# Kernel optimization log

Hardware: AMD Instinct MI355X
Metric: run time of the kernel (lower is better)

## Reference

```python
import jax, jax.numpy as jnp
import numpy as np

B, T, C, H = 4, 2048, 1024, 16
D = C // H  # head_size = 64

def setup_inputs() -> dict:
    key = jax.random.key(0)
    ks = jax.random.split(key, 9)
    s = 1.0 / np.sqrt(C)
    return {
        "x":  jax.random.normal(ks[0], (B, T, C), dtype=jnp.float32),
        "Wq": jax.random.normal(ks[1], (C, C), dtype=jnp.float32) * s,
        "bq": jnp.zeros((C,), dtype=jnp.float32),
        "Wk": jax.random.normal(ks[2], (C, C), dtype=jnp.float32) * s,
        "bk": jnp.zeros((C,), dtype=jnp.float32),
        "Wv": jax.random.normal(ks[3], (C, C), dtype=jnp.float32) * s,
        "bv": jnp.zeros((C,), dtype=jnp.float32),
        "Wp": jax.random.normal(ks[4], (C, C), dtype=jnp.float32) * s,
        "bp": jnp.zeros((C,), dtype=jnp.float32),
    }

def reference(x, Wq, bq, Wk, bk, Wv, bv, Wp, bp):
    # projections -> [B, H, T, D]
    def split_heads(y):
        return y.reshape(B, T, H, D).transpose(0, 2, 1, 3)
    q = split_heads(x @ Wq + bq)
    k = split_heads(x @ Wk + bk)
    v = split_heads(x @ Wv + bv)
    scale = 1.0 / np.sqrt(D)
    att = jnp.einsum('bhqd,bhkd->bhqk', q, k) * scale  # [B,H,T,T]
    causal = jnp.tril(jnp.ones((T, T), dtype=bool))
    att = jnp.where(causal, att, -jnp.inf)
    att = jax.nn.softmax(att, axis=-1)
    # dropout p=0.0 (eval): identity
    y = jnp.einsum('bhqk,bhkd->bhqd', att, v)  # [B,H,T,D]
    y = y.transpose(0, 2, 1, 3).reshape(B, T, C)
    return y @ Wp + bp
```

## Files before the change

kernel.cpp:

```cpp
#include <hip/hip_runtime.h>
#include <hip/hip_bf16.h>

#define B_ 4
#define T_ 2048
#define C_ 1024
#define H_ 16
#define D_ 64
#define M_ (B_*T_)

typedef __bf16 bf16x8 __attribute__((ext_vector_type(8)));
typedef float  f32x4  __attribute__((ext_vector_type(4)));
typedef float  f32x16 __attribute__((ext_vector_type(16)));

__device__ __forceinline__ unsigned short f2bf(float f) {
  unsigned u = __builtin_bit_cast(unsigned, f);
  u += 0x7FFF + ((u >> 16) & 1);
  return (unsigned short)(u >> 16);
}

__device__ __forceinline__ float exp2fast(float x) {
#if __has_builtin(__builtin_amdgcn_exp2f)
  return __builtin_amdgcn_exp2f(x);
#else
  float r; asm("v_exp_f32 %0, %1" : "=v"(r) : "v"(x)); return r;
#endif
}

__device__ __forceinline__ void gload_lds16(const void* g, void* l) {
  __builtin_amdgcn_global_load_lds(
      (const __attribute__((address_space(1))) void*)g,
      (__attribute__((address_space(3))) void*)l, 16, 0, 0);
}

__global__ void cvt_f32_bf16(const float* __restrict__ in,
                             unsigned short* __restrict__ out, int n4) {
  int i = blockIdx.x * blockDim.x + threadIdx.x;
  if (i < n4) {
    float4 v = ((const float4*)in)[i];
    ushort4 o;
    o.x = f2bf(v.x); o.y = f2bf(v.y); o.z = f2bf(v.z); o.w = f2bf(v.w);
    ((ushort4*)out)[i] = o;
  }
}

__global__ void transpose_cvt(const float* __restrict__ w0, const float* __restrict__ w1,
                              const float* __restrict__ w2, const float* __restrict__ w3,
                              unsigned short* __restrict__ tqkv,
                              unsigned short* __restrict__ tp) {
  __shared__ float tile[32][33];
  const float* src; unsigned short* dst;
  switch (blockIdx.z) {
    case 0: src = w0; dst = tqkv; break;
    case 1: src = w1; dst = tqkv + (size_t)C_ * C_; break;
    case 2: src = w2; dst = tqkv + (size_t)2 * C_ * C_; break;
    default: src = w3; dst = tp; break;
  }
  int bx = blockIdx.x * 32;
  int by = blockIdx.y * 32;
  int tx = threadIdx.x, ty = threadIdx.y;
  #pragma unroll
  for (int j = 0; j < 4; ++j)
    tile[ty + 8*j][tx] = src[(size_t)(by + ty + 8*j) * C_ + bx + tx];
  __syncthreads();
  #pragma unroll
  for (int j = 0; j < 4; ++j)
    dst[(size_t)(bx + ty + 8*j) * C_ + by + tx] = f2bf(tile[tx][ty + 8*j]);
}

__global__ __launch_bounds__(256, 2)
void gemm_qkv(const unsigned short* __restrict__ A,
              const unsigned short* __restrict__ Bt,
              const float* __restrict__ bq, const float* __restrict__ bk,
              const float* __restrict__ bv,
              unsigned short* __restrict__ qout, unsigned short* __restrict__ kout,
              unsigned short* __restrict__ vout, float qscale)
{
  __shared__ unsigned short lsA[128 * 64];
  __shared__ unsigned short lsB[128 * 64];
  const int wave = threadIdx.x >> 6;
  const int lane = threadIdx.x & 63;
  const int rowBase = blockIdx.y * 128;
  const int colBase = blockIdx.x * 128;
  const int rowOff = (wave >> 1) * 64;
  const int colOff = (wave & 1) * 64;
  const int lr = lane & 15;
  const int lg = lane >> 4;

  f32x4 acc[4][4] = {};

  const int chunkRow = lane >> 3;
  const int srcColE  = (((lane & 7) ^ (lane >> 3)) * 8);

  for (int k0 = 0; k0 < C_; k0 += 64) {
    #pragma unroll
    for (int c = 0; c < 4; ++c) {
      int chunk = c * 4 + wave;
      int r = chunk * 8 + chunkRow;
      gload_lds16(A  + (size_t)(rowBase + r) * C_ + k0 + srcColE, &lsA[chunk * 512]);
      gload_lds16(Bt + (size_t)(colBase + r) * C_ + k0 + srcColE, &lsB[chunk * 512]);
    }
    __syncthreads();
    #pragma unroll
    for (int kk = 0; kk < 2; ++kk) {
      bf16x8 af[4], bfr[4];
      const int kbyte = (kk * 32 + lg * 8) * 2;
      #pragma unroll
      for (int m = 0; m < 4; ++m) {
        int row = rowOff + m * 16 + lr;
        af[m] = *(const bf16x8*)((const char*)lsA + row * 128 + (kbyte ^ ((row & 7) << 4)));
      }
      #pragma unroll
      for (int n = 0; n < 4; ++n) {
        int row = colOff + n * 16 + lr;
        bfr[n] = *(const bf16x8*)((const char*)lsB + row * 128 + (kbyte ^ ((row & 7) << 4)));
      }
      #pragma unroll
      for (int m = 0; m < 4; ++m)
        #pragma unroll
        for (int n = 0; n < 4; ++n)
          acc[m][n] = __builtin_amdgcn_mfma_f32_16x16x32_bf16(af[m], bfr[n], acc[m][n], 0, 0, 0);
    }
    __syncthreads();
  }

  const int mid = colBase >> 10;
  const float* bias = (mid == 0) ? bq : (mid == 1) ? bk : bv;
  const float oscale = (mid == 0) ? qscale : 1.f;
  unsigned short* outp = (mid == 0) ? qout : (mid == 1) ? kout : vout;

  #pragma unroll
  for (int m = 0; m < 4; ++m) {
    int row0 = rowBase + rowOff + m * 16 + lg * 4;
    #pragma unroll
    for (int n = 0; n < 4; ++n) {
      int col = colBase + colOff + n * 16 + lr;
      int ncol = col & 1023;
      float bs = bias[ncol];
      int h = ncol >> 6, d = ncol & 63;
      if (mid == 2) {
        int b = row0 >> 11, t = row0 & 2047;
        int t2 = (t & ~12) | ((t & 4) << 1) | ((t & 8) >> 1);
        ushort4 o;
        o.x = f2bf(acc[m][n][0] + bs);
        o.y = f2bf(acc[m][n][1] + bs);
        o.z = f2bf(acc[m][n][2] + bs);
        o.w = f2bf(acc[m][n][3] + bs);
        *(ushort4*)(outp + (((size_t)b * H_ + h) * D_ + d) * T_ + t2) = o;
      } else {
        #pragma unroll
        for (int j = 0; j < 4; ++j) {
          int r = row0 + j;
          int b = r >> 11, t = r & 2047;
          outp[((((size_t)b * H_ + h) * T_ + t) << 6) + d] = f2bf((acc[m][n][j] + bs) * oscale);
        }
      }
    }
  }
}

__global__ __launch_bounds__(256, 2)
void gemm_proj(const unsigned short* __restrict__ A,
               const unsigned short* __restrict__ Bt,
               const float* __restrict__ bias,
               float* __restrict__ Cout)
{
  __shared__ unsigned short lsA[128 * 64];
  __shared__ unsigned short lsB[128 * 64];
  const int wave = threadIdx.x >> 6;
  const int lane = threadIdx.x & 63;
  const int rowBase = blockIdx.y * 128;
  const int colBase = blockIdx.x * 128;
  const int rowOff = (wave >> 1) * 64;
  const int colOff = (wave & 1) * 64;
  const int lr = lane & 15;
  const int lg = lane >> 4;

  f32x4 acc[4][4] = {};

  const int chunkRow = lane >> 3;
  const int srcColE  = (((lane & 7) ^ (lane >> 3)) * 8);

  for (int k0 = 0; k0 < C_; k0 += 64) {
    #pragma unroll
    for (int c = 0; c < 4; ++c) {
      int chunk = c * 4 + wave;
      int r = chunk * 8 + chunkRow;
      gload_lds16(A  + (size_t)(rowBase + r) * C_ + k0 + srcColE, &lsA[chunk * 512]);
      gload_lds16(Bt + (size_t)(colBase + r) * C_ + k0 + srcColE, &lsB[chunk * 512]);
    }
    __syncthreads();
    #pragma unroll
    for (int kk = 0; kk < 2; ++kk) {
      bf16x8 af[4], bfr[4];
      const int kbyte = (kk * 32 + lg * 8) * 2;
      #pragma unroll
      for (int m = 0; m < 4; ++m) {
        int row = rowOff + m * 16 + lr;
        af[m] = *(const bf16x8*)((const char*)lsA + row * 128 + (kbyte ^ ((row & 7) << 4)));
      }
      #pragma unroll
      for (int n = 0; n < 4; ++n) {
        int row = colOff + n * 16 + lr;
        bfr[n] = *(const bf16x8*)((const char*)lsB + row * 128 + (kbyte ^ ((row & 7) << 4)));
      }
      #pragma unroll
      for (int m = 0; m < 4; ++m)
        #pragma unroll
        for (int n = 0; n < 4; ++n)
          acc[m][n] = __builtin_amdgcn_mfma_f32_16x16x32_bf16(af[m], bfr[n], acc[m][n], 0, 0, 0);
    }
    __syncthreads();
  }

  #pragma unroll
  for (int m = 0; m < 4; ++m) {
    int row0 = rowBase + rowOff + m * 16 + lg * 4;
    #pragma unroll
    for (int n = 0; n < 4; ++n) {
      int col = colBase + colOff + n * 16 + lr;
      float bs = bias[col];
      #pragma unroll
      for (int j = 0; j < 4; ++j)
        Cout[(size_t)(row0 + j) * C_ + col] = acc[m][n][j] + bs;
    }
  }
}

__global__ __launch_bounds__(256, 2)
void attn12(const unsigned short* __restrict__ q,
            const unsigned short* __restrict__ k,
            const unsigned short* __restrict__ vp,
            unsigned short* __restrict__ y)
{
  __shared__ unsigned short lsK[3][64 * 64];
  __shared__ unsigned short lsV[2][64 * 64];
  const int tid  = threadIdx.x;
  const int wave = tid >> 6;
  const int lane = tid & 63;
  const int col  = lane & 31;
  const int hi   = lane >> 5;

  const int bid = blockIdx.x;
  const int xcd = bid & 7;
  const int idx = bid >> 3;
  const int bh  = xcd * 8 + (idx & 7);
  const int ss  = 15 - (idx >> 3);
  const int b = bh >> 4, h = bh & 15;

  const unsigned short* qh = q  + (size_t)bh * T_ * D_;
  const unsigned short* kh = k  + (size_t)bh * T_ * D_;
  const unsigned short* vh = vp + (size_t)bh * D_ * T_;

  const int srow = tid >> 3;
  const int srcE = ((tid & 7) * 8) ^ ((srow & 7) << 3);
  const unsigned short* ksrc = kh + srow * D_ + srcE;
  const unsigned short* vsrc = vh + srow * T_ + srcE;

  const int swz = (col & 7) << 4;
  const f32x16 zc = {};

  const int q0 = ss * 128 + wave * 32;
  const int nsteps = 2 * ss + 2;

  bf16x8 bqf[4];
  {
    const unsigned short* qrow = qh + (size_t)(q0 + col) * D_ + hi * 8;
    #pragma unroll
    for (int ks = 0; ks < 4; ++ks) bqf[ks] = *(const bf16x8*)(qrow + ks * 16);
  }

  f32x16 ot0 = {}, ot1 = {};
  float m = -INFINITY, l = 0.f;
  bf16x8 pf0, pf1, pf2, pf3;

  auto STAGEK = [&](int t) {
    unsigned short* bK = &lsK[0][0] + (t % 3) * 4096;
    const unsigned short* kg = ksrc + (size_t)t * 64 * D_;
    gload_lds16(kg,           bK + tid * 8);
    gload_lds16(kg + 32 * D_, bK + (tid + 256) * 8);
  };
  auto STAGEV = [&](int t) {
    unsigned short* bV = &lsV[0][0] + (t & 1) * 4096;
    const unsigned short* vg = vsrc + t * 64;
    gload_lds16(vg,           bV + tid * 8);
    gload_lds16(vg + 32 * T_, bV + (tid + 256) * 8);
  };

  STAGEK(0);
  STAGEV(0);
  STAGEK(1);

  for (int s = 0; s < nsteps; ++s) {
    if (s + 1 < nsteps) {
      asm volatile("s_waitcnt vmcnt(2)" ::: "memory");
    } else {
      asm volatile("s_waitcnt vmcnt(0)" ::: "memory");
    }
    __builtin_amdgcn_s_barrier();
    __builtin_amdgcn_sched_barrier(0);
    if (s + 1 < nsteps) STAGEV(s + 1);
    if (s + 2 < nsteps) STAGEK(s + 2);

    const int n0 = s * 64;
    if (n0 <= q0 + 31) {
      const bool two = (n0 < q0);
      const unsigned short* baseK = &lsK[0][0] + (s % 3) * 4096;
      const unsigned short* baseV = &lsV[0][0] + (s & 1) * 4096;
      f32x16 st0, st1;
      {
        const char* kb0 = (const char*)baseK + col * 128;
        __builtin_amdgcn_s_setprio(1);
        st0 = __builtin_amdgcn_mfma_f32_32x32x16_bf16(
                *(const bf16x8*)(kb0 + ((0 * 32 + hi * 16) ^ swz)), bqf[0], zc, 0, 0, 0);
        st0 = __builtin_amdgcn_mfma_f32_32x32x16_bf16(
                *(const bf16x8*)(kb0 + ((1 * 32 + hi * 16) ^ swz)), bqf[1], st0, 0, 0, 0);
        st0 = __builtin_amdgcn_mfma_f32_32x32x16_bf16(
                *(const bf16x8*)(kb0 + ((2 * 32 + hi * 16) ^ swz)), bqf[2], st0, 0, 0, 0);
        st0 = __builtin_amdgcn_mfma_f32_32x32x16_bf16(
                *(const bf16x8*)(kb0 + ((3 * 32 + hi * 16) ^ swz)), bqf[3], st0, 0, 0, 0);
        if (two) {
          const char* kb1 = kb0 + 32 * 128;
          f32x16 a;
          a = __builtin_amdgcn_mfma_f32_32x32x16_bf16(
                *(const bf16x8*)(kb1 + ((0 * 32 + hi * 16) ^ swz)), bqf[0], zc, 0, 0, 0);
          a = __builtin_amdgcn_mfma_f32_32x32x16_bf16(
                *(const bf16x8*)(kb1 + ((1 * 32 + hi * 16) ^ swz)), bqf[1], a, 0, 0, 0);
          a = __builtin_amdgcn_mfma_f32_32x32x16_bf16(
                *(const bf16x8*)(kb1 + ((2 * 32 + hi * 16) ^ swz)), bqf[2], a, 0, 0, 0);
          a = __builtin_amdgcn_mfma_f32_32x32x16_bf16(
                *(const bf16x8*)(kb1 + ((3 * 32 + hi * 16) ^ swz)), bqf[3], a, 0, 0, 0);
          st1 = a;
        }
        __builtin_amdgcn_s_setprio(0);
      }
      if (n0 + 63 > q0) {
        #pragma unroll
        for (int rr = 0; rr < 16; ++rr) {
          int key0 = n0 + (rr & 3) + 8 * (rr >> 2) + 4 * hi;
          if (key0 > q0 + col) st0[rr] = -INFINITY;
          if (two) { if (key0 + 32 > q0 + col) st1[rr] = -INFINITY; }
        }
      }
      float mm;
      {
        float a0 = fmaxf(fmaxf(st0[0], st0[1]), fmaxf(st0[2], st0[3]));
        float a1 = fmaxf(fmaxf(st0[4], st0[5]), fmaxf(st0[6], st0[7]));
        float a2 = fmaxf(fmaxf(st0[8], st0[9]), fmaxf(st0[10], st0[11]));
        float a3 = fmaxf(fmaxf(st0[12], st0[13]), fmaxf(st0[14], st0[15]));
        if (two) {
          a0 = fmaxf(a0, fmaxf(fmaxf(st1[0], st1[1]), fmaxf(st1[2], st1[3])));
          a1 = fmaxf(a1, fmaxf(fmaxf(st1[4], st1[5]), fmaxf(st1[6], st1[7])));
          a2 = fmaxf(a2, fmaxf(fmaxf(st1[8], st1[9]), fmaxf(st1[10], st1[11])));
          a3 = fmaxf(a3, fmaxf(fmaxf(st1[12], st1[13]), fmaxf(st1[14], st1[15])));
        }
        mm = fmaxf(fmaxf(a0, a1), fmaxf(a2, a3));
      }
      if (!__all(mm <= m + 8.f)) {
        float mf = fmaxf(mm, __shfl_xor(mm, 32));
        float mnew = fmaxf(m, mf);
        float corr = exp2fast(m - mnew);
        m = mnew;
        l *= corr;
        #pragma unroll
        for (int rr = 0; rr < 16; ++rr) { ot0[rr] *= corr; ot1[rr] *= corr; }
      }
      {
        float pa[8];
        bf16x8 w;
        #pragma unroll
        for (int e = 0; e < 8; ++e) { pa[e] = exp2fast(st0[e] - m); w[e] = (__bf16)pa[e]; }
        pf0 = w;
        l += ((pa[0] + pa[1]) + (pa[2] + pa[3])) + ((pa[4] + pa[5]) + (pa[6] + pa[7]));
      }
      {
        float pb[8];
        bf16x8 w;
        #pragma unroll
        for (int e = 0; e < 8; ++e) { pb[e] = exp2fast(st0[8 + e] - m); w[e] = (__bf16)pb[e]; }
        pf1 = w;
        l += ((pb[0] + pb[1]) + (pb[2] + pb[3])) + ((pb[4] + pb[5]) + (pb[6] + pb[7]));
      }
      if (two) {
        float pa[8];
        bf16x8 w;
        #pragma unroll
        for (int e = 0; e < 8; ++e) { pa[e] = exp2fast(st1[e] - m); w[e] = (__bf16)pa[e]; }
        pf2 = w;
        l += ((pa[0] + pa[1]) + (pa[2] + pa[3])) + ((pa[4] + pa[5]) + (pa[6] + pa[7]));
        float pb[8];
        #pragma unroll
        for (int e = 0; e < 8; ++e) { pb[e] = exp2fast(st1[8 + e] - m); w[e] = (__bf16)pb[e]; }
        pf3 = w;
        l += ((pb[0] + pb[1]) + (pb[2] + pb[3])) + ((pb[4] + pb[5]) + (pb[6] + pb[7]));
      }
      {
        const char* vb0 = (const char*)baseV + col * 128;
        const char* vb1 = vb0 + 32 * 128;
        __builtin_amdgcn_s_setprio(1);
        #pragma unroll
        for (int ks = 0; ks < 2; ++ks) {
          bf16x8 pw = ks ? pf1 : pf0;
          bf16x8 av0 = *(const bf16x8*)(vb0 + ((ks * 32 + hi * 16) ^ swz));
          bf16x8 av1 = *(const bf16x8*)(vb1 + ((ks * 32 + hi * 16) ^ swz));
          ot0 = __builtin_amdgcn_mfma_f32_32x32x16_bf16(av0, pw, ot0, 0, 0, 0);
          ot1 = __builtin_amdgcn_mfma_f32_32x32x16_bf16(av1, pw, ot1, 0, 0, 0);
        }
        if (two) {
          #pragma unroll
          for (int ks = 2; ks < 4; ++ks) {
            bf16x8 pw = (ks == 3) ? pf3 : pf2;
            bf16x8 av0 = *(const bf16x8*)(vb0 + ((ks * 32 + hi * 16) ^ swz));
            bf16x8 av1 = *(const bf16x8*)(vb1 + ((ks * 32 + hi * 16) ^ swz));
            ot0 = __builtin_amdgcn_mfma_f32_32x32x16_bf16(av0, pw, ot0, 0, 0, 0);
            ot1 = __builtin_amdgcn_mfma_f32_32x32x16_bf16(av1, pw, ot1, 0, 0, 0);
          }
        }
        __builtin_amdgcn_s_setprio(0);
      }
    }
    __builtin_amdgcn_sched_barrier(0);
  }

  float lf = l + __shfl_xor(l, 32);
  float inv = 1.f / lf;
  unsigned short* yrow = y + ((size_t)b * T_ + q0 + col) * C_ + h * D_;
  #pragma unroll
  for (int a = 0; a < 4; ++a) {
    ushort4 o4;
    o4.x = f2bf(ot0[4 * a + 0] * inv);
    o4.y = f2bf(ot0[4 * a + 1] * inv);
    o4.z = f2bf(ot0[4 * a + 2] * inv);
    o4.w = f2bf(ot0[4 * a + 3] * inv);
    *(ushort4*)(yrow + 8 * a + 4 * hi) = o4;
  }
  #pragma unroll
  for (int a = 0; a < 4; ++a) {
    ushort4 o4;
    o4.x = f2bf(ot1[4 * a + 0] * inv);
    o4.y = f2bf(ot1[4 * a + 1] * inv);
    o4.z = f2bf(ot1[4 * a + 2] * inv);
    o4.w = f2bf(ot1[4 * a + 3] * inv);
    *(ushort4*)(yrow + 32 + 8 * a + 4 * hi) = o4;
  }
}

extern "C" void kernel_launch(void* const* d_in, const int* in_sizes, int n_in,
                              void* d_out, int out_size, void* d_ws, size_t ws_size,
                              hipStream_t stream) {
  const float* x  = (const float*)d_in[0];
  const float* Wq = (const float*)d_in[1];
  const float* bq = (const float*)d_in[2];
  const float* Wk = (const float*)d_in[3];
  const float* bk = (const float*)d_in[4];
  const float* Wv = (const float*)d_in[5];
  const float* bv = (const float*)d_in[6];
  const float* Wp = (const float*)d_in[7];
  const float* bp = (const float*)d_in[8];
  float* out = (float*)d_out;

  char* ws = (char*)d_ws;
  unsigned short* xb    = (unsigned short*)ws; ws += (size_t)M_ * C_ * 2;
  unsigned short* wqkvt = (unsigned short*)ws; ws += (size_t)3 * C_ * C_ * 2;
  unsigned short* wpt   = (unsigned short*)ws; ws += (size_t)C_ * C_ * 2;
  unsigned short* qb    = (unsigned short*)ws; ws += (size_t)M_ * C_ * 2;
  unsigned short* kb    = (unsigned short*)ws; ws += (size_t)M_ * C_ * 2;
  unsigned short* vtb   = (unsigned short*)ws; ws += (size_t)M_ * C_ * 2;
  unsigned short* yb    = (unsigned short*)ws; ws += (size_t)M_ * C_ * 2;

  cvt_f32_bf16<<<dim3((M_ * C_ / 4 + 255) / 256), dim3(256), 0, stream>>>(x, xb, M_ * C_ / 4);
  transpose_cvt<<<dim3(32, 32, 4), dim3(32, 8), 0, stream>>>(Wq, Wk, Wv, Wp, wqkvt, wpt);

  const float qscale = 0.125f * 1.4426950408889634f;
  gemm_qkv<<<dim3(3 * C_ / 128, M_ / 128), dim3(256), 0, stream>>>(
      xb, wqkvt, bq, bk, bv, qb, kb, vtb, qscale);

  attn12<<<dim3(1024), dim3(256), 0, stream>>>(qb, kb, vtb, yb);

  gemm_proj<<<dim3(C_ / 128, M_ / 128), dim3(256), 0, stream>>>(yb, wpt, bp, out);
}
```

Measured before the change: 159.2 us.

## Software-pipeline attention: overlap QK^T of next tile with softmax/PV of previous

Restructures the attention loop so that each iteration computes the QK^T MFMAs for tile s while finishing the softmax and PV MFMAs for tile s-1. Score tiles ping-pong between two register sets, and V staging is shifted one step later to match. The intent is to hide the latency of the exp/max work behind matrix-core work within a wave. The cost is another 32 live accumulator registers, which could reduce occupancy or cause spills under the 2-blocks launch bound.

```diff
diff --git a/kernel.cpp b/kernel.cpp
--- a/kernel.cpp
+++ b/kernel.cpp
@@ -227,7 +227,7 @@
 }
 
 __global__ __launch_bounds__(256, 2)
-void attn12(const unsigned short* __restrict__ q,
+void attn13(const unsigned short* __restrict__ q,
             const unsigned short* __restrict__ k,
             const unsigned short* __restrict__ vp,
             unsigned short* __restrict__ y)
@@ -271,7 +271,7 @@
 
   f32x16 ot0 = {}, ot1 = {};
   float m = -INFINITY, l = 0.f;
-  bf16x8 pf0, pf1, pf2, pf3;
+  f32x16 SA0, SA1, SB0, SB1;
 
   auto STAGEK = [&](int t) {
     unsigned short* bK = &lsK[0][0] + (t % 3) * 4096;
@@ -286,140 +286,145 @@
     gload_lds16(vg + 32 * T_, bV + (tid + 256) * 8);
   };
 
+  auto FINISH = [&](int t, f32x16& SP0, f32x16& SP1) {
+    const int n0 = t * 64;
+    const bool two = (n0 < q0);
+    if (n0 + 63 > q0) {
+      #pragma unroll
+      for (int rr = 0; rr < 16; ++rr) {
+        int key0 = n0 + (rr & 3) + 8 * (rr >> 2) + 4 * hi;
+        if (key0 > q0 + col) SP0[rr] = -INFINITY;
+        if (two) { if (key0 + 32 > q0 + col) SP1[rr] = -INFINITY; }
+      }
+    }
+    float mm;
+    {
+      float a0 = fmaxf(fmaxf(SP0[0], SP0[1]), fmaxf(SP0[2], SP0[3]));
+      float a1 = fmaxf(fmaxf(SP0[4], SP0[5]), fmaxf(SP0[6], SP0[7]));
+      float a2 = fmaxf(fmaxf(SP0[8], SP0[9]), fmaxf(SP0[10], SP0[11]));
+      float a3 = fmaxf(fmaxf(SP0[12], SP0[13]), fmaxf(SP0[14], SP0[15]));
+      if (two) {
+        a0 = fmaxf(a0, fmaxf(fmaxf(SP1[0], SP1[1]), fmaxf(SP1[2], SP1[3])));
+        a1 = fmaxf(a1, fmaxf(fmaxf(SP1[4], SP1[5]), fmaxf(SP1[6], SP1[7])));
+        a2 = fmaxf(a2, fmaxf(fmaxf(SP1[8], SP1[9]), fmaxf(SP1[10], SP1[11])));
+        a3 = fmaxf(a3, fmaxf(fmaxf(SP1[12], SP1[13]), fmaxf(SP1[14], SP1[15])));
+      }
+      mm = fmaxf(fmaxf(a0, a1), fmaxf(a2, a3));
+    }
+    if (!__all(mm <= m + 8.f)) {
+      float mf = fmaxf(mm, __shfl_xor(mm, 32));
+      float mnew = fmaxf(m, mf);
+      float corr = exp2fast(m - mnew);
+      m = mnew;
+      l *= corr;
+      #pragma unroll
+      for (int rr = 0; rr < 16; ++rr) { ot0[rr] *= corr; ot1[rr] *= corr; }
+    }
+    bf16x8 pf0, pf1, pf2, pf3;
+    {
+      float pa[8];
+      bf16x8 w;
+      #pragma unroll
+      for (int e = 0; e < 8; ++e) { pa[e] = exp2fast(SP0[e] - m); w[e] = (__bf16)pa[e]; }
+      pf0 = w;
+      l += ((pa[0] + pa[1]) + (pa[2] + pa[3])) + ((pa[4] + pa[5]) + (pa[6] + pa[7]));
+    }
+    {
+      float pb[8];
+      bf16x8 w;
+      #pragma unroll
+      for (int e = 0; e < 8; ++e) { pb[e] = exp2fast(SP0[8 + e] - m); w[e] = (__bf16)pb[e]; }
+      pf1 = w;
+      l += ((pb[0] + pb[1]) + (pb[2] + pb[3])) + ((pb[4] + pb[5]) + (pb[6] + pb[7]));
+    }
+    if (two) {
+      float pa[8];
+      bf16x8 w;
+      #pragma unroll
+      for (int e = 0; e < 8; ++e) { pa[e] = exp2fast(SP1[e] - m); w[e] = (__bf16)pa[e]; }
+      pf2 = w;
+      l += ((pa[0] + pa[1]) + (pa[2] + pa[3])) + ((pa[4] + pa[5]) + (pa[6] + pa[7]));
+      float pb[8];
+      #pragma unroll
+      for (int e = 0; e < 8; ++e) { pb[e] = exp2fast(SP1[8 + e] - m); w[e] = (__bf16)pb[e]; }
+      pf3 = w;
+      l += ((pb[0] + pb[1]) + (pb[2] + pb[3])) + ((pb[4] + pb[5]) + (pb[6] + pb[7]));
+    }
+    const char* vb0 = (const char*)(&lsV[0][0] + (t & 1) * 4096) + col * 128;
+    const char* vb1 = vb0 + 32 * 128;
+    __builtin_amdgcn_s_setprio(1);
+    #pragma unroll
+    for (int ks = 0; ks < 2; ++ks) {
+      bf16x8 pw = ks ? pf1 : pf0;
+      bf16x8 av0 = *(const bf16x8*)(vb0 + ((ks * 32 + hi * 16) ^ swz));
+      bf16x8 av1 = *(const bf16x8*)(vb1 + ((ks * 32 + hi * 16) ^ swz));
+      ot0 = __builtin_amdgcn_mfma_f32_32x32x16_bf16(av0, pw, ot0, 0, 0, 0);
+      ot1 = __builtin_amdgcn_mfma_f32_32x32x16_bf16(av1, pw, ot1, 0, 0, 0);
+    }
+    if (two) {
+      #pragma unroll
+      for (int ks = 2; ks < 4; ++ks) {
+        bf16x8 pw = (ks == 3) ? pf3 : pf2;
+        bf16x8 av0 = *(const bf16x8*)(vb0 + ((ks * 32 + hi * 16) ^ swz));
+        bf16x8 av1 = *(const bf16x8*)(vb1 + ((ks * 32 + hi * 16) ^ swz));
+        ot0 = __builtin_amdgcn_mfma_f32_32x32x16_bf16(av0, pw, ot0, 0, 0, 0);
+        ot1 = __builtin_amdgcn_mfma_f32_32x32x16_bf16(av1, pw, ot1, 0, 0, 0);
+      }
+    }
+    __builtin_amdgcn_s_setprio(0);
+  };
+
   STAGEK(0);
-  STAGEV(0);
   STAGEK(1);
 
-  for (int s = 0; s < nsteps; ++s) {
-    if (s + 1 < nsteps) {
-      asm volatile("s_waitcnt vmcnt(2)" ::: "memory");
-    } else {
-      asm volatile("s_waitcnt vmcnt(0)" ::: "memory");
-    }
-    __builtin_amdgcn_s_barrier();
-    __builtin_amdgcn_sched_barrier(0);
-    if (s + 1 < nsteps) STAGEV(s + 1);
-    if (s + 2 < nsteps) STAGEK(s + 2);
-
-    const int n0 = s * 64;
-    if (n0 <= q0 + 31) {
-      const bool two = (n0 < q0);
-      const unsigned short* baseK = &lsK[0][0] + (s % 3) * 4096;
-      const unsigned short* baseV = &lsV[0][0] + (s & 1) * 4096;
-      f32x16 st0, st1;
-      {
-        const char* kb0 = (const char*)baseK + col * 128;
-        __builtin_amdgcn_s_setprio(1);
-        st0 = __builtin_amdgcn_mfma_f32_32x32x16_bf16(
-                *(const bf16x8*)(kb0 + ((0 * 32 + hi * 16) ^ swz)), bqf[0], zc, 0, 0, 0);
-        st0 = __builtin_amdgcn_mfma_f32_32x32x16_bf16(
-                *(const bf16x8*)(kb0 + ((1 * 32 + hi * 16) ^ swz)), bqf[1], st0, 0, 0, 0);
-        st0 = __builtin_amdgcn_mfma_f32_32x32x16_bf16(
-                *(const bf16x8*)(kb0 + ((2 * 32 + hi * 16) ^ swz)), bqf[2], st0, 0, 0, 0);
-        st0 = __builtin_amdgcn_mfma_f32_32x32x16_bf16(
-                *(const bf16x8*)(kb0 + ((3 * 32 + hi * 16) ^ swz)), bqf[3], st0, 0, 0, 0);
-        if (two) {
-          const char* kb1 = kb0 + 32 * 128;
-          f32x16 a;
-          a = __builtin_amdgcn_mfma_f32_32x32x16_bf16(
-                *(const bf16x8*)(kb1 + ((0 * 32 + hi * 16) ^ swz)), bqf[0], zc, 0, 0, 0);
-          a = __builtin_amdgcn_mfma_f32_32x32x16_bf16(
-                *(const bf16x8*)(kb1 + ((1 * 32 + hi * 16) ^ swz)), bqf[1], a, 0, 0, 0);
-          a = __builtin_amdgcn_mfma_f32_32x32x16_bf16(
-                *(const bf16x8*)(kb1 + ((2 * 32 + hi * 16) ^ swz)), bqf[2], a, 0, 0, 0);
-          a = __builtin_amdgcn_mfma_f32_32x32x16_bf16(
-                *(const bf16x8*)(kb1 + ((3 * 32 + hi * 16) ^ swz)), bqf[3], a, 0, 0, 0);
-          st1 = a;
-        }
-        __builtin_amdgcn_s_setprio(0);
-      }
-      if (n0 + 63 > q0) {
-        #pragma unroll
-        for (int rr = 0; rr < 16; ++rr) {
-          int key0 = n0 + (rr & 3) + 8 * (rr >> 2) + 4 * hi;
-          if (key0 > q0 + col) st0[rr] = -INFINITY;
-          if (two) { if (key0 + 32 > q0 + col) st1[rr] = -INFINITY; }
-        }
-      }
-      float mm;
-      {
-        float a0 = fmaxf(fmaxf(st0[0], st0[1]), fmaxf(st0[2], st0[3]));
-        float a1 = fmaxf(fmaxf(st0[4], st0[5]), fmaxf(st0[6], st0[7]));
-        float a2 = fmaxf(fmaxf(st0[8], st0[9]), fmaxf(st0[10], st0[11]));
-        float a3 = fmaxf(fmaxf(st0[12], st0[13]), fmaxf(st0[14], st0[15]));
-        if (two) {
-          a0 = fmaxf(a0, fmaxf(fmaxf(st1[0], st1[1]), fmaxf(st1[2], st1[3])));
-          a1 = fmaxf(a1, fmaxf(fmaxf(st1[4], st1[5]), fmaxf(st1[6], st1[7])));
-          a2 = fmaxf(a2, fmaxf(fmaxf(st1[8], st1[9]), fmaxf(st1[10], st1[11])));
-          a3 = fmaxf(a3, fmaxf(fmaxf(st1[12], st1[13]), fmaxf(st1[14], st1[15])));
-        }
-        mm = fmaxf(fmaxf(a0, a1), fmaxf(a2, a3));
-      }
-      if (!__all(mm <= m + 8.f)) {
-        float mf = fmaxf(mm, __shfl_xor(mm, 32));
-        float mnew = fmaxf(m, mf);
-        float corr = exp2fast(m - mnew);
-        m = mnew;
-        l *= corr;
-        #pragma unroll
-        for (int rr = 0; rr < 16; ++rr) { ot0[rr] *= corr; ot1[rr] *= corr; }
-      }
-      {
-        float pa[8];
-        bf16x8 w;
-        #pragma unroll
-        for (int e = 0; e < 8; ++e) { pa[e] = exp2fast(st0[e] - m); w[e] = (__bf16)pa[e]; }
-        pf0 = w;
-        l += ((pa[0] + pa[1]) + (pa[2] + pa[3])) + ((pa[4] + pa[5]) + (pa[6] + pa[7]));
-      }
-      {
-        float pb[8];
-        bf16x8 w;
-        #pragma unroll
-        for (int e = 0; e < 8; ++e) { pb[e] = exp2fast(st0[8 + e] - m); w[e] = (__bf16)pb[e]; }
-        pf1 = w;
-        l += ((pb[0] + pb[1]) + (pb[2] + pb[3])) + ((pb[4] + pb[5]) + (pb[6] + pb[7]));
-      }
-      if (two) {
-        float pa[8];
-        bf16x8 w;
-        #pragma unroll
-        for (int e = 0; e < 8; ++e) { pa[e] = exp2fast(st1[e] - m); w[e] = (__bf16)pa[e]; }
-        pf2 = w;
-        l += ((pa[0] + pa[1]) + (pa[2] + pa[3])) + ((pa[4] + pa[5]) + (pa[6] + pa[7]));
-        float pb[8];
-        #pragma unroll
-        for (int e = 0; e < 8; ++e) { pb[e] = exp2fast(st1[8 + e] - m); w[e] = (__bf16)pb[e]; }
-        pf3 = w;
-        l += ((pb[0] + pb[1]) + (pb[2] + pb[3])) + ((pb[4] + pb[5]) + (pb[6] + pb[7]));
-      }
-      {
-        const char* vb0 = (const char*)baseV + col * 128;
-        const char* vb1 = vb0 + 32 * 128;
-        __builtin_amdgcn_s_setprio(1);
-        #pragma unroll
-        for (int ks = 0; ks < 2; ++ks) {
-          bf16x8 pw = ks ? pf1 : pf0;
-          bf16x8 av0 = *(const bf16x8*)(vb0 + ((ks * 32 + hi * 16) ^ swz));
-          bf16x8 av1 = *(const bf16x8*)(vb1 + ((ks * 32 + hi * 16) ^ swz));
-          ot0 = __builtin_amdgcn_mfma_f32_32x32x16_bf16(av0, pw, ot0, 0, 0, 0);
-          ot1 = __builtin_amdgcn_mfma_f32_32x32x16_bf16(av1, pw, ot1, 0, 0, 0);
-        }
-        if (two) {
-          #pragma unroll
-          for (int ks = 2; ks < 4; ++ks) {
-            bf16x8 pw = (ks == 3) ? pf3 : pf2;
-            bf16x8 av0 = *(const bf16x8*)(vb0 + ((ks * 32 + hi * 16) ^ swz));
-            bf16x8 av1 = *(const bf16x8*)(vb1 + ((ks * 32 + hi * 16) ^ swz));
-            ot0 = __builtin_amdgcn_mfma_f32_32x32x16_bf16(av0, pw, ot0, 0, 0, 0);
-            ot1 = __builtin_amdgcn_mfma_f32_32x32x16_bf16(av1, pw, ot1, 0, 0, 0);
-          }
-        }
-        __builtin_amdgcn_s_setprio(0);
-      }
-    }
-    __builtin_amdgcn_sched_barrier(0);
-  }
+  int s = 0;
+
+#define ITER(SN0, SN1)                                                              \
+  do {                                                                              \
+    if (s + 1 < nsteps) { asm volatile("s_waitcnt vmcnt(2)" ::: "memory"); }        \
+    else               { asm volatile("s_waitcnt vmcnt(0)" ::: "memory"); }         \
+    __builtin_amdgcn_s_barrier();                                                   \
+    __builtin_amdgcn_sched_barrier(0);                                              \
+    if (s < nsteps) STAGEV(s);                                                      \
+    if (s + 2 < nsteps) STAGEK(s + 2);                                              \
+    if (s < nsteps && s * 64 <= q0 + 31) {                                          \
+      const char* kb0 = (const char*)(&lsK[0][0] + (s % 3) * 4096) + col * 128;     \
+      __builtin_amdgcn_s_setprio(1);                                                \
+      SN0 = __builtin_amdgcn_mfma_f32_32x32x16_bf16(                                \
+              *(const bf16x8*)(kb0 + ((0 * 32 + hi * 16) ^ swz)), bqf[0], zc, 0, 0, 0); \
+      SN0 = __builtin_amdgcn_mfma_f32_32x32x16_bf16(                                \
+              *(const bf16x8*)(kb0 + ((1 * 32 + hi * 16) ^ swz)), bqf[1], SN0, 0, 0, 0); \
+      SN0 = __builtin_amdgcn_mfma_f32_32x32x16_bf16(                                \
+              *(const bf16x8*)(kb0 + ((2 * 32 + hi * 16) ^ swz)), bqf[2], SN0, 0, 0, 0); \
+      SN0 = __builtin_amdgcn_mfma_f32_32x32x16_bf16(                                \
+              *(const bf16x8*)(kb0 + ((3 * 32 + hi * 16) ^ swz)), bqf[3], SN0, 0, 0, 0); \
+      if (s * 64 < q0) {                                                            \
+        const char* kb1 = kb0 + 32 * 128;                                           \
+        f32x16 a;                                                                   \
+        a = __builtin_amdgcn_mfma_f32_32x32x16_bf16(                                \
+              *(const bf16x8*)(kb1 + ((0 * 32 + hi * 16) ^ swz)), bqf[0], zc, 0, 0, 0); \
+        a = __builtin_amdgcn_mfma_f32_32x32x16_bf16(                                \
+              *(const bf16x8*)(kb1 + ((1 * 32 + hi * 16) ^ swz)), bqf[1], a, 0, 0, 0); \
+        a = __builtin_amdgcn_mfma_f32_32x32x16_bf16(                                \
+              *(const bf16x8*)(kb1 + ((2 * 32 + hi * 16) ^ swz)), bqf[2], a, 0, 0, 0); \
+        a = __builtin_amdgcn_mfma_f32_32x32x16_bf16(                                \
+              *(const bf16x8*)(kb1 + ((3 * 32 + hi * 16) ^ swz)), bqf[3], a, 0, 0, 0); \
+        SN1 = a;                                                                    \
+      }                                                                             \
+      __builtin_amdgcn_s_setprio(0);                                                \
+    }                                                                               \
+    if (s >= 1 && (s - 1) * 64 <= q0 + 31)                                          \
+      FINISH(s - 1, (s & 1) ? SA0 : SB0, (s & 1) ? SA1 : SB1);                      \
+    __builtin_amdgcn_sched_barrier(0);                                              \
+  } while (0)
+
+  while (true) {
+    ITER(SA0, SA1);
+    if (++s > nsteps) break;
+    ITER(SB0, SB1);
+    if (++s > nsteps) break;
+  }
+#undef ITER
 
   float lf = l + __shfl_xor(l, 32);
   float inv = 1.f / lf;
@@ -474,7 +479,7 @@
   gemm_qkv<<<dim3(3 * C_ / 128, M_ / 128), dim3(256), 0, stream>>>(
       xb, wqkvt, bq, bk, bv, qb, kb, vtb, qscale);
 
-  attn12<<<dim3(1024), dim3(256), 0, stream>>>(qb, kb, vtb, yb);
+  attn13<<<dim3(1024), dim3(256), 0, stream>>>(qb, kb, vtb, yb);
 
   gemm_proj<<<dim3(C_ / 128, M_ / 128), dim3(256), 0, stream>>>(yb, wpt, bp, out);
 }
```

Result: slower. 168.6 us (+5.9%).
